# Optimization experiments

Measured on AMD Instinct MI355X. Metric: run time of the kernel, lower is better.

## Reference

```python
import jax, jax.numpy as jnp
import numpy as np

B, L, T, H, NH, NQ = 4096, 64, 48, 64, 4, 3
HD = H // NH  # head dim = 16


def lstm_layer(x, h0, c0, Wih, Whh, bih, bhh):
    # x: (B, S, I); h0, c0: (B, H). PyTorch gate order: i, f, g, o.
    def step(carry, xt):
        h, c = carry
        g = xt @ Wih.T + bih + h @ Whh.T + bhh
        i, f, gg, o = jnp.split(g, 4, axis=-1)
        c = jax.nn.sigmoid(f) * c + jax.nn.sigmoid(i) * jnp.tanh(gg)
        h = jax.nn.sigmoid(o) * jnp.tanh(c)
        return (h, c), h
    (hT, cT), hs = jax.lax.scan(step, (h0, c0), jnp.swapaxes(x, 0, 1))
    return jnp.swapaxes(hs, 0, 1), hT, cT


def lstm2(x, params, h0, c0):
    # params: list of 2 tuples (Wih, Whh, bih, bhh); h0, c0: (2, B, H)
    out = x
    hs, cs = [], []
    for l in range(2):
        Wih, Whh, bih, bhh = params[l]
        out, h, c = lstm_layer(out, h0[l], c0[l], Wih, Whh, bih, bhh)
        hs.append(h)
        cs.append(c)
    return out, jnp.stack(hs), jnp.stack(cs)


def mha(q, k, v, Wqkv, bqkv, Wo, bo):
    # PyTorch nn.MultiheadAttention, batch_first, averaged attn weights.
    Wq, Wk, Wv = jnp.split(Wqkv, 3, axis=0)
    bq, bk, bv = jnp.split(bqkv, 3, axis=0)
    def heads(t):
        b, s, _ = t.shape
        return t.reshape(b, s, NH, HD)
    qh = heads(q @ Wq.T + bq)
    kh = heads(k @ Wk.T + bk)
    vh = heads(v @ Wv.T + bv)
    scores = jnp.einsum('bqhd,bkhd->bhqk', qh, kh) / jnp.sqrt(jnp.float32(HD))
    w = jax.nn.softmax(scores, axis=-1)                      # (B, NH, Sq, Sk)
    out = jnp.einsum('bhqk,bkhd->bqhd', w, vh).reshape(q.shape[0], q.shape[1], H)
    return out @ Wo.T + bo, w.mean(axis=1)                   # averaged over heads


def setup_inputs() -> dict:
    key = jax.random.key(0)
    ks = iter(jax.random.split(key, 32))
    s = 0.08
    d = {
        'x': jax.random.normal(next(ks), (B, L, H), jnp.float32),
        'target': jax.random.normal(next(ks), (B, T, H), jnp.float32),
    }
    for pre in ('enc', 'dec'):
        for l in range(2):
            d[f'{pre}_Wih{l}'] = jax.random.normal(next(ks), (4 * H, H), jnp.float32) * s
            d[f'{pre}_Whh{l}'] = jax.random.normal(next(ks), (4 * H, H), jnp.float32) * s
            d[f'{pre}_bih{l}'] = jnp.zeros((4 * H,), jnp.float32)
            d[f'{pre}_bhh{l}'] = jnp.zeros((4 * H,), jnp.float32)
    d['attn_Wqkv'] = jax.random.normal(next(ks), (3 * H, H), jnp.float32) * s
    d['attn_bqkv'] = jnp.zeros((3 * H,), jnp.float32)
    d['attn_Wo'] = jax.random.normal(next(ks), (H, H), jnp.float32) * s
    d['attn_bo'] = jnp.zeros((H,), jnp.float32)
    d['fc_W1'] = jax.random.normal(next(ks), (H // 2, H), jnp.float32) * s
    d['fc_b1'] = jnp.zeros((H // 2,), jnp.float32)
    d['fc_W2'] = jax.random.normal(next(ks), (NQ, H // 2), jnp.float32) * s
    d['fc_b2'] = jnp.zeros((NQ,), jnp.float32)
    return d


def reference(x, target,
              enc_Wih0, enc_Whh0, enc_bih0, enc_bhh0,
              enc_Wih1, enc_Whh1, enc_bih1, enc_bhh1,
              dec_Wih0, dec_Whh0, dec_bih0, dec_bhh0,
              dec_Wih1, dec_Whh1, dec_bih1, dec_bhh1,
              attn_Wqkv, attn_bqkv, attn_Wo, attn_bo,
              fc_W1, fc_b1, fc_W2, fc_b2):
    enc_p = [(enc_Wih0, enc_Whh0, enc_bih0, enc_bhh0),
             (enc_Wih1, enc_Whh1, enc_bih1, enc_bhh1)]
    dec_p = [(dec_Wih0, dec_Whh0, dec_bih0, dec_bhh0),
             (dec_Wih1, dec_Whh1, dec_bih1, dec_bhh1)]
    z = jnp.zeros((2, x.shape[0], H), x.dtype)
    enc_out, h_n, c_n = lstm2(x, enc_p, z, z)               # (B, L, H)
    attn0, _ = mha(enc_out, enc_out, enc_out, attn_Wqkv, attn_bqkv, attn_Wo, attn_bo)
    # teacher forcing: step t>=1 consumes target[:, t-1]; step 0 the attended encoder summary
    dec_in = jnp.concatenate([attn0[:, -1:, :], target[:, :-1, :]], axis=1)  # (B, T, H)
    dec_out, _, _ = lstm2(dec_in, dec_p, h_n, c_n)          # (B, T, H)
    attn_out, attn_w = mha(dec_out, enc_out, enc_out, attn_Wqkv, attn_bqkv, attn_Wo, attn_bo)
    pred = jax.nn.relu(attn_out @ fc_W1.T + fc_b1) @ fc_W2.T + fc_b2  # (B, T, 3)
    return pred, attn_w                                      # (B,T,3), (B,T,L)
```

## Files before the change

### kernel.cpp

```cpp
#include <hip/hip_runtime.h>
#include <hip/hip_bf16.h>
#include <cstddef>


#define B_   4096
#define L_   64
#define T_   48
#define H_   64
#define ROWS 16
#define PADH 136
#define PADH2 72

using half8  = __attribute__((ext_vector_type(8))) _Float16;
using half4  = __attribute__((ext_vector_type(4))) _Float16;
using f32x4  = __attribute__((ext_vector_type(4))) float;

#define IC_ 4.8828125e-4f

__device__ __forceinline__ float fsig(float x) {
    return __builtin_amdgcn_rcpf(1.0f + __expf(-x));
}
__device__ __forceinline__ float ftanh(float x) {
    float e = __expf(-2.0f * fabsf(x));
    float r = (1.0f - e) * __builtin_amdgcn_rcpf(1.0f + e);
    return copysignf(r, x);
}

__global__ void transpose_w_all_kernel(
    const float* __restrict__ W0i, const float* __restrict__ W0h,
    const float* __restrict__ W1i, const float* __restrict__ W1h,
    const float* __restrict__ W2i, const float* __restrict__ W2h,
    const float* __restrict__ W3i, const float* __restrict__ W3h,
    _Float16* __restrict__ out) {
    int idx = blockIdx.x * 256 + threadIdx.x;
    int layer = idx >> 14, i = idx & 16383;
    const float* Wi = (layer == 0) ? W0i : (layer == 1) ? W1i : (layer == 2) ? W2i : W3i;
    const float* Wh = (layer == 0) ? W0h : (layer == 1) ? W1h : (layer == 2) ? W2h : W3h;
    int r = i >> 6, k = i & 63;
    _Float16* o = out + (size_t)layer * 32768;
    o[r * 128 + k]      = (_Float16)Wi[i];
    o[r * 128 + 64 + k] = (_Float16)Wh[i];
}

__global__ void split_aux_kernel(const float* __restrict__ Wqkv,
                                 const float* __restrict__ Wo,
                                 const float* __restrict__ W1,
                                 _Float16* __restrict__ wqkvh,
                                 _Float16* __restrict__ woh,
                                 _Float16* __restrict__ w1h,
                                 float* __restrict__ woT) {
    int idx = blockIdx.x * 256 + threadIdx.x;
    if (idx < 12288) {
        float v = Wqkv[idx]; _Float16 h = (_Float16)v;
        wqkvh[idx] = h; wqkvh[12288 + idx] = (_Float16)((v - (float)h) * 2048.f);
    } else if (idx < 16384) {
        int i = idx - 12288;
        float v = Wo[i]; _Float16 h = (_Float16)v;
        woh[i] = h; woh[4096 + i] = (_Float16)((v - (float)h) * 2048.f);
    } else if (idx < 18432) {
        int i = idx - 16384;
        float v = W1[i]; _Float16 h = (_Float16)v;
        w1h[i] = h; w1h[2048 + i] = (_Float16)((v - (float)h) * 2048.f);
    } else if (idx < 22528) {
        int i = idx - 18432; int r = i >> 6, k = i & 63;
        woT[k * 64 + r] = Wo[i];
    }
}

__global__ __launch_bounds__(512, 2) void lstm2_mfma_kernel(
    const float* __restrict__ inseq,
    const float* __restrict__ in0,
    const _Float16* __restrict__ w1half,
    const float* __restrict__ b1ihp, const float* __restrict__ b1hhp,
    const _Float16* __restrict__ w2half,
    const float* __restrict__ b2ihp, const float* __restrict__ b2hhp,
    const float* __restrict__ h01, const float* __restrict__ c01,
    const float* __restrict__ h02, const float* __restrict__ c02,
    _Float16* __restrict__ outh2,
    float* __restrict__ hf1, float* __restrict__ cf1,
    float* __restrict__ hf2, float* __restrict__ cf2,
    int S, int mode)
{
    __shared__ __align__(16) _Float16 A1[2][16 * PADH];
    __shared__ __align__(16) _Float16 A2h[2][16 * PADH2];

    const int tid  = threadIdx.x;
    const int w    = tid >> 6;
    const int lrow = tid & 15;
    const int lkg  = (tid >> 4) & 3;
    const int row0 = blockIdx.x * ROWS;

    const bool isL2w = (w >= 4);
    const int  wl    = w & 3;
    const int  hcol  = wl * 16 + lrow;

    const _Float16* wsrc = isL2w ? w2half : w1half;
    const float* bihp = isL2w ? b2ihp : b1ihp;
    const float* bhhp = isL2w ? b2hhp : b1hhp;

    half8 whi[4][4];
    #pragma unroll
    for (int kt = 0; kt < 4; ++kt)
        #pragma unroll
        for (int g = 0; g < 4; ++g) {
            const int col = g * 64 + hcol;
            whi[kt][g] = *(const half8*)&wsrc[(size_t)col * 128 + kt * 32 + lkg * 8];
        }
    float bsv[4];
    #pragma unroll
    for (int g = 0; g < 4; ++g)
        bsv[g] = bihp[g * 64 + hcol] + bhhp[g * 64 + hcol];

    float c[4], hlast[4] = {0.f, 0.f, 0.f, 0.f};

    const float* px[4];
    _Float16*    ph[4];

    if (!isL2w) {
        #pragma unroll
        for (int q = 0; q < 4; ++q) {
            const int r = 4 * lkg + q;
            const float* p0 = (mode == 1) ? (in0 + (size_t)(row0 + r) * 64)
                                          : (inseq + (size_t)(row0 + r) * S * 64);
            A1[0][r * PADH + hcol] = (_Float16)p0[hcol];
            float hv = h01 ? h01[(size_t)(row0 + r) * 64 + hcol] : 0.f;
            A1[0][r * PADH + 64 + hcol] = (_Float16)hv;
            c[q] = c01 ? c01[(size_t)(row0 + r) * 64 + hcol] : 0.f;
            px[q] = inseq + (size_t)(row0 + r) * S * 64 + hcol
                  + (mode == 1 ? 0 : 64);
        }
    } else {
        #pragma unroll
        for (int q = 0; q < 4; ++q) {
            const int r = 4 * lkg + q;
            float hv = h02 ? h02[(size_t)(row0 + r) * 64 + hcol] : 0.f;
            A2h[0][r * PADH2 + hcol] = (_Float16)hv;
            c[q] = c02 ? c02[(size_t)(row0 + r) * 64 + hcol] : 0.f;
            ph[q] = outh2 + (size_t)(row0 + r) * S * 64 + hcol;
        }
    }

    const int aoff = lrow * PADH + lkg * 8;

    for (int i = 0; i <= S; ++i) {
        asm volatile("s_waitcnt lgkmcnt(0)" ::: "memory");
        __builtin_amdgcn_s_barrier();
        __builtin_amdgcn_sched_barrier(0);

        if (!isL2w) {
            if (i < S) {
                float xn[4];
                if (i + 1 < S) {
                    #pragma unroll
                    for (int q = 0; q < 4; ++q) { xn[q] = *px[q]; px[q] += 64; }
                }
                const _Float16* As = A1[i & 1];
                f32x4 a0[4];
                #pragma unroll
                for (int g = 0; g < 4; ++g)
                    a0[g] = (f32x4){bsv[g], bsv[g], bsv[g], bsv[g]};
                #pragma unroll
                for (int kt = 0; kt < 4; ++kt) {
                    half8 ah = *(const half8*)&As[aoff + kt * 32];
                    #pragma unroll
                    for (int g = 0; g < 4; ++g)
                        a0[g] = __builtin_amdgcn_mfma_f32_16x16x32_f16(ah, whi[kt][g], a0[g], 0, 0, 0);
                }
                _Float16* Ad1 = A1[(i + 1) & 1];
                #pragma unroll
                for (int q = 0; q < 4; ++q) {
                    const int r = 4 * lkg + q;
                    float gi = a0[0][q], gf = a0[1][q], gg = a0[2][q], go = a0[3][q];
                    c[q] = fsig(gf) * c[q] + fsig(gi) * ftanh(gg);
                    float hv = fsig(go) * ftanh(c[q]);
                    hlast[q] = hv;
                    Ad1[r * PADH + 64 + hcol] = (_Float16)hv;
                }
                if (i + 1 < S) {
                    #pragma unroll
                    for (int q = 0; q < 4; ++q) {
                        const int r = 4 * lkg + q;
                        Ad1[r * PADH + hcol] = (_Float16)xn[q];
                    }
                }
            }
        } else {
            const int j = i - 1;
            if (j >= 0 && j < S) {
                const _Float16* Ah1 = A1[(j + 1) & 1];
                const _Float16* Ah2 = A2h[j & 1];
                f32x4 a0[4];
                #pragma unroll
                for (int g = 0; g < 4; ++g)
                    a0[g] = (f32x4){bsv[g], bsv[g], bsv[g], bsv[g]};
                #pragma unroll
                for (int kt = 0; kt < 2; ++kt) {
                    half8 ah = *(const half8*)&Ah1[lrow * PADH + 64 + kt * 32 + lkg * 8];
                    #pragma unroll
                    for (int g = 0; g < 4; ++g)
                        a0[g] = __builtin_amdgcn_mfma_f32_16x16x32_f16(ah, whi[kt][g], a0[g], 0, 0, 0);
                }
                #pragma unroll
                for (int kt = 2; kt < 4; ++kt) {
                    half8 ah = *(const half8*)&Ah2[lrow * PADH2 + (kt - 2) * 32 + lkg * 8];
                    #pragma unroll
                    for (int g = 0; g < 4; ++g)
                        a0[g] = __builtin_amdgcn_mfma_f32_16x16x32_f16(ah, whi[kt][g], a0[g], 0, 0, 0);
                }
                _Float16* Ad = A2h[(j + 1) & 1];
                #pragma unroll
                for (int q = 0; q < 4; ++q) {
                    const int r = 4 * lkg + q;
                    float gi = a0[0][q], gf = a0[1][q], gg = a0[2][q], go = a0[3][q];
                    c[q] = fsig(gf) * c[q] + fsig(gi) * ftanh(gg);
                    float hv = fsig(go) * ftanh(c[q]);
                    hlast[q] = hv;
                    _Float16 hh = (_Float16)hv;
                    Ad[r * PADH2 + hcol] = hh;
                    *ph[q] = hh; ph[q] += 64;
                }
            }
        }
    }
    if (hf1) {
        float* hdst = isL2w ? hf2 : hf1;
        float* cdst = isL2w ? cf2 : cf1;
        #pragma unroll
        for (int q = 0; q < 4; ++q) {
            const int r = 4 * lkg + q;
            hdst[(size_t)(row0 + r) * 64 + hcol] = hlast[q];
            cdst[(size_t)(row0 + r) * 64 + hcol] = c[q];
        }
    }
}

__global__ __launch_bounds__(256, 4) void attn0_v2(
    const _Float16* __restrict__ ench,
    const _Float16* __restrict__ wqkvh,
    const float* __restrict__ bqkv,
    const float* __restrict__ woT,
    const float* __restrict__ bo,
    float* __restrict__ a0last)
{
    __shared__ __align__(16) _Float16 E[64 * 72];
    __shared__ __align__(16) _Float16 K[64 * 72];
    __shared__ __align__(16) _Float16 V[64 * 72];
    __shared__ __align__(16) _Float16 Q[64 * 72];
    __shared__ float wsm[4 * 68];
    __shared__ float ov[64];
    __shared__ float part[4 * 64];

    const int b = blockIdx.x, tid = threadIdx.x;
    const int w = tid >> 6, l = tid & 63, lr = l & 15, lkg = l >> 4;

    {
        int row = tid >> 2, c0 = (tid & 3) * 16;
        const _Float16* ep = ench + (size_t)b * 4096 + row * 64 + c0;
        *(half8*)&E[row * 72 + c0]     = *(const half8*)ep;
        *(half8*)&E[row * 72 + c0 + 8] = *(const half8*)(ep + 8);
    }
    __syncthreads();

    for (int tt = w; tt < 12; tt += 4) {
        const int kind = tt >> 2;
        const int mrow = (tt & 3) * 16;
        const int wrowB = (kind == 0) ? 64 : ((kind == 1) ? 128 : 0);
        half8 ah[2];
        #pragma unroll
        for (int kt = 0; kt < 2; ++kt)
            ah[kt] = *(const half8*)&E[(mrow + lr) * 72 + kt * 32 + lkg * 8];
        _Float16* dst = (kind == 0) ? K : ((kind == 1) ? V : Q);
        #pragma unroll
        for (int nt = 0; nt < 4; ++nt) {
            const int col = nt * 16 + lr;
            const float bv = bqkv[wrowB + col];
            f32x4 a0 = (f32x4){bv, bv, bv, bv};
            #pragma unroll
            for (int kt = 0; kt < 2; ++kt) {
                half8 bh = *(const half8*)&wqkvh[(size_t)(wrowB + col) * 64 + kt * 32 + lkg * 8];
                a0 = __builtin_amdgcn_mfma_f32_16x16x32_f16(ah[kt], bh, a0, 0, 0, 0);
            }
            #pragma unroll
            for (int i = 0; i < 4; ++i)
                dst[(mrow + lkg * 4 + i) * 72 + col] = (_Float16)a0[i];
        }
    }
    __syncthreads();

    {
        const int kv = l;
        float s = 0.f;
        #pragma unroll
        for (int d = 0; d < 16; ++d)
            s += (float)Q[63 * 72 + w * 16 + d] * (float)K[kv * 72 + w * 16 + d];
        s *= 0.25f;
        float m = s;
        #pragma unroll
        for (int off = 32; off; off >>= 1) m = fmaxf(m, __shfl_xor(m, off));
        float e = __expf(s - m);
        float sum = e;
        #pragma unroll
        for (int off = 32; off; off >>= 1) sum += __shfl_xor(sum, off);
        wsm[w * 68 + kv] = e / sum;
    }
    __syncthreads();

    {
        const int d = l & 15, gr = l >> 4;
        float o = 0.f;
        #pragma unroll
        for (int k = 0; k < 16; ++k) {
            const int kv = gr * 16 + k;
            o += wsm[w * 68 + kv] * (float)V[kv * 72 + w * 16 + d];
        }
        o += __shfl_xor(o, 16);
        o += __shfl_xor(o, 32);
        if (l < 16) ov[w * 16 + l] = o;
    }
    __syncthreads();

    {
        const int j = tid & 63, g = tid >> 6;
        float p = 0.f;
        #pragma unroll
        for (int k = 0; k < 16; ++k) {
            const int kk = g * 16 + k;
            p += ov[kk] * woT[kk * 64 + j];
        }
        part[g * 64 + j] = p;
    }
    __syncthreads();
    if (tid < 64) {
        float a = bo[tid] + part[tid] + part[64 + tid] + part[128 + tid] + part[192 + tid];
        a0last[(size_t)b * 64 + tid] = a;
    }
}

__global__ __launch_bounds__(256, 4) void cross_attn_v3(
    const _Float16* __restrict__ ench, const _Float16* __restrict__ dech,
    const _Float16* __restrict__ wqkvh, const float* __restrict__ bqkv,
    const _Float16* __restrict__ woh,   const float* __restrict__ bo,
    const _Float16* __restrict__ w1h,   const float* __restrict__ b1,
    const float* __restrict__ W2,       const float* __restrict__ b2,
    float* __restrict__ pred, float* __restrict__ attnw)
{
    extern __shared__ __align__(16) char smem[];
    _Float16* E  = (_Float16*)(smem);
    _Float16* D  = (_Float16*)(smem + 9216);
    _Float16* K  = (_Float16*)(smem + 16128);
    _Float16* Q  = (_Float16*)(smem + 25344);
    _Float16* VT = (_Float16*)(smem + 32256);
    _Float16* AO = (_Float16*)(smem + 32256);
    float*    Hl = (float*)(smem + 32256);

    const int b = blockIdx.x, tid = threadIdx.x;
    const int w = tid >> 6, l = tid & 63, lr = l & 15, lkg = l >> 4;
    const int h = w;

    {
        int row = tid >> 2, c0 = (tid & 3) * 16;
        const _Float16* ep = ench + (size_t)b * 4096 + row * 64 + c0;
        *(half8*)&E[row * 72 + c0]     = *(const half8*)ep;
        *(half8*)&E[row * 72 + c0 + 8] = *(const half8*)(ep + 8);
        if (row < 48) {
            const _Float16* dp = dech + (size_t)b * 3072 + row * 64 + c0;
            *(half8*)&D[row * 72 + c0]     = *(const half8*)dp;
            *(half8*)&D[row * 72 + c0 + 8] = *(const half8*)(dp + 8);
        }
    }
    __syncthreads();

    for (int tt = w; tt < 11; tt += 4) {
        const int kind = (tt < 4) ? 0 : ((tt < 8) ? 1 : 2);
        const int mrow = ((kind == 0) ? tt : (kind == 1) ? tt - 4 : tt - 8) * 16;
        const int wrowB = (kind == 0) ? 64 : ((kind == 1) ? 128 : 0);
        const _Float16* S = (kind == 2) ? D : E;
        half8 ah[2];
        #pragma unroll
        for (int kt = 0; kt < 2; ++kt)
            ah[kt] = *(const half8*)&S[(mrow + lr) * 72 + kt * 32 + lkg * 8];
        #pragma unroll
        for (int nt = 0; nt < 4; ++nt) {
            const int col = nt * 16 + lr;
            const float bv = bqkv[wrowB + col];
            f32x4 a0 = (f32x4){bv, bv, bv, bv};
            #pragma unroll
            for (int kt = 0; kt < 2; ++kt) {
                half8 bh = *(const half8*)&wqkvh[(size_t)(wrowB + col) * 64 + kt * 32 + lkg * 8];
                a0 = __builtin_amdgcn_mfma_f32_16x16x32_f16(ah[kt], bh, a0, 0, 0, 0);
            }
            if (kind == 1) {
                half4 p;
                #pragma unroll
                for (int i = 0; i < 4; ++i) p[i] = (_Float16)a0[i];
                *(half4*)&VT[col * 68 + mrow + lkg * 4] = p;
            } else {
                _Float16* dst = (kind == 0) ? K : Q;
                #pragma unroll
                for (int i = 0; i < 4; ++i)
                    dst[(mrow + lkg * 4 + i) * 72 + col] = (_Float16)a0[i];
            }
        }
    }
    __syncthreads();

    const half8 z = {0, 0, 0, 0, 0, 0, 0, 0};
    half8 ka[4], qb[3];
    #pragma unroll
    for (int kvt = 0; kvt < 4; ++kvt)
        ka[kvt] = (lkg < 2) ? *(const half8*)&K[(kvt * 16 + lr) * 72 + h * 16 + lkg * 8] : z;
    #pragma unroll
    for (int qt = 0; qt < 3; ++qt)
        qb[qt] = (lkg < 2) ? *(const half8*)&Q[(qt * 16 + lr) * 72 + h * 16 + lkg * 8] : z;
    __syncthreads();

    _Float16* strip = (_Float16*)(smem + ((h == 0) ? 0 : (h == 1) ? 9216
                                        : (h == 2) ? 16128 : 25344));
    {
        f32x4 s[3][4];
        #pragma unroll
        for (int qt = 0; qt < 3; ++qt) {
            #pragma unroll
            for (int kvt = 0; kvt < 4; ++kvt) {
                f32x4 a0 = (f32x4){0.f, 0.f, 0.f, 0.f};
                a0 = __builtin_amdgcn_mfma_f32_16x16x32_f16(ka[kvt], qb[qt], a0, 0, 0, 0);
                s[qt][kvt] = a0 * 0.25f;
            }
            float m = s[qt][0][0];
            #pragma unroll
            for (int kvt = 0; kvt < 4; ++kvt)
                #pragma unroll
                for (int i = 0; i < 4; ++i) m = fmaxf(m, s[qt][kvt][i]);
            m = fmaxf(m, __shfl_xor(m, 16));
            m = fmaxf(m, __shfl_xor(m, 32));
            float sum = 0.f;
            #pragma unroll
            for (int kvt = 0; kvt < 4; ++kvt)
                #pragma unroll
                for (int i = 0; i < 4; ++i) {
                    float e = __expf(s[qt][kvt][i] - m);
                    s[qt][kvt][i] = e;
                    sum += e;
                }
            sum += __shfl_xor(sum, 16);
            sum += __shfl_xor(sum, 32);
            const float r = 1.0f / sum;
            #pragma unroll
            for (int kvt = 0; kvt < 4; ++kvt) {
                half4 p;
                #pragma unroll
                for (int i = 0; i < 4; ++i) p[i] = (_Float16)(s[qt][kvt][i] * r);
                *(half4*)&strip[(qt * 16 + lr) * 72 + kvt * 16 + lkg * 4] = p;
            }
        }
    }
    f32x4 pv[3];
    {
        half8 vb[2];
        #pragma unroll
        for (int kt = 0; kt < 2; ++kt) {
            half4 lo4 = *(const half4*)&VT[(h * 16 + lr) * 68 + kt * 32 + lkg * 8];
            half4 hi4 = *(const half4*)&VT[(h * 16 + lr) * 68 + kt * 32 + lkg * 8 + 4];
            #pragma unroll
            for (int j = 0; j < 4; ++j) { vb[kt][j] = lo4[j]; vb[kt][4 + j] = hi4[j]; }
        }
        #pragma unroll
        for (int qt = 0; qt < 3; ++qt) {
            f32x4 acc = (f32x4){0.f, 0.f, 0.f, 0.f};
            #pragma unroll
            for (int kt = 0; kt < 2; ++kt) {
                half8 wa = *(const half8*)&strip[(qt * 16 + lr) * 72 + kt * 32 + lkg * 8];
                acc = __builtin_amdgcn_mfma_f32_16x16x32_f16(wa, vb[kt], acc, 0, 0, 0);
            }
            pv[qt] = acc;
        }
    }
    __syncthreads();

    #pragma unroll
    for (int qt = 0; qt < 3; ++qt)
        #pragma unroll
        for (int i = 0; i < 4; ++i)
            AO[(qt * 16 + lkg * 4 + i) * 72 + h * 16 + lr] = (_Float16)pv[qt][i];
    __syncthreads();

    if (w < 3) {
        half8 bAO[2];
        #pragma unroll
        for (int kt = 0; kt < 2; ++kt)
            bAO[kt] = *(const half8*)&AO[(w * 16 + lr) * 72 + kt * 32 + lkg * 8];
        f32x4 ov[4];
        #pragma unroll
        for (int nt = 0; nt < 4; ++nt) {
            f32x4 acc = *(const f32x4*)&bo[nt * 16 + lkg * 4];
            #pragma unroll
            for (int kt = 0; kt < 2; ++kt) {
                half8 aW = *(const half8*)&woh[(size_t)(nt * 16 + lr) * 64 + kt * 32 + lkg * 8];
                acc = __builtin_amdgcn_mfma_f32_16x16x32_f16(aW, bAO[kt], acc, 0, 0, 0);
            }
            ov[nt] = acc;
        }
        #pragma unroll
        for (int nt = 0; nt < 4; ++nt) {
            half4 p;
            #pragma unroll
            for (int i = 0; i < 4; ++i) p[i] = (_Float16)ov[nt][i];
            *(half4*)&AO[(w * 16 + lr) * 72 + nt * 16 + lkg * 4] = p;
        }
        half8 bO[2];
        #pragma unroll
        for (int kt = 0; kt < 2; ++kt)
            bO[kt] = *(const half8*)&AO[(w * 16 + lr) * 72 + kt * 32 + lkg * 8];
        #pragma unroll
        for (int nt = 0; nt < 2; ++nt) {
            f32x4 acc = *(const f32x4*)&b1[nt * 16 + lkg * 4];
            #pragma unroll
            for (int kt = 0; kt < 2; ++kt) {
                half8 aW = *(const half8*)&w1h[(size_t)(nt * 16 + lr) * 64 + kt * 32 + lkg * 8];
                acc = __builtin_amdgcn_mfma_f32_16x16x32_f16(aW, bO[kt], acc, 0, 0, 0);
            }
            f32x4 rl;
            #pragma unroll
            for (int i = 0; i < 4; ++i) rl[i] = fmaxf(acc[i], 0.f);
            *(f32x4*)&Hl[(w * 16 + lr) * 36 + nt * 16 + lkg * 4] = rl;
        }
        if (l < 48) {
            const int qr = l / 3, n = l - 3 * qr;
            const int q = w * 16 + qr;
            float a = b2[n];
            #pragma unroll
            for (int m2 = 0; m2 < 32; ++m2) a += Hl[q * 36 + m2] * W2[n * 32 + m2];
            pred[((size_t)b * 48 + q) * 3 + n] = a;
        }
    } else {
        const _Float16* s0 = (const _Float16*)(smem);
        const _Float16* s1 = (const _Float16*)(smem + 9216);
        const _Float16* s2 = (const _Float16*)(smem + 16128);
        const _Float16* s3 = (const _Float16*)(smem + 25344);
        #pragma unroll 4
        for (int it = 0; it < 48; ++it) {
            int idx = l + it * 64;
            int o = (idx >> 6) * 72 + (idx & 63);
            attnw[(size_t)b * 3072 + idx] =
                0.25f * ((float)s0[o] + (float)s1[o] + (float)s2[o] + (float)s3[o]);
        }
    }
}

extern "C" void kernel_launch(void* const* d_in, const int* in_sizes, int n_in,
                              void* d_out, int out_size, void* d_ws, size_t ws_size,
                              hipStream_t stream) {
    const float* x      = (const float*)d_in[0];
    const float* target = (const float*)d_in[1];
    const float* eWih0 = (const float*)d_in[2],  *eWhh0 = (const float*)d_in[3];
    const float* ebih0 = (const float*)d_in[4],  *ebhh0 = (const float*)d_in[5];
    const float* eWih1 = (const float*)d_in[6],  *eWhh1 = (const float*)d_in[7];
    const float* ebih1 = (const float*)d_in[8],  *ebhh1 = (const float*)d_in[9];
    const float* dWih0 = (const float*)d_in[10], *dWhh0 = (const float*)d_in[11];
    const float* dbih0 = (const float*)d_in[12], *dbhh0 = (const float*)d_in[13];
    const float* dWih1 = (const float*)d_in[14], *dWhh1 = (const float*)d_in[15];
    const float* dbih1 = (const float*)d_in[16], *dbhh1 = (const float*)d_in[17];
    const float* Wqkv = (const float*)d_in[18], *bqkv = (const float*)d_in[19];
    const float* Wo   = (const float*)d_in[20], *bo   = (const float*)d_in[21];
    const float* W1   = (const float*)d_in[22], *b1   = (const float*)d_in[23];
    const float* W2   = (const float*)d_in[24], *b2   = (const float*)d_in[25];

    float* ws = (float*)d_ws;
    float* hseq1  = ws;
    float* encout = hseq1  + (size_t)B_ * L_ * H_;
    float* decout = encout + (size_t)B_ * L_ * H_;
    float* a0last = decout + (size_t)B_ * T_ * H_;
    float* hfin   = a0last + (size_t)B_ * H_;
    float* cfin   = hfin   + (size_t)2 * B_ * H_;
    float* wtg    = cfin   + (size_t)2 * B_ * H_;
    float* auxw   = wtg    + (size_t)4 * 32768;

    _Float16* wh0 = (_Float16*)(wtg);
    _Float16* wh1 = wh0 + 32768;
    _Float16* wh2 = wh1 + 32768;
    _Float16* wh3 = wh2 + 32768;
    _Float16* wqkvh = (_Float16*)auxw;
    _Float16* woh   = wqkvh + 24576;
    _Float16* w1h   = woh + 8192;
    float*    woT   = auxw + 18432;
    _Float16* encouth = (_Float16*)hseq1;
    _Float16* decouth = encouth + (size_t)B_ * L_ * H_;

    float* pred  = (float*)d_out;
    float* attnw = pred + (size_t)B_ * T_ * 3;

    transpose_w_all_kernel<<<256, 256, 0, stream>>>(
        eWih0, eWhh0, eWih1, eWhh1, dWih0, dWhh0, dWih1, dWhh1, wh0);
    split_aux_kernel<<<88, 256, 0, stream>>>(Wqkv, Wo, W1, wqkvh, woh, w1h, woT);

    lstm2_mfma_kernel<<<B_ / ROWS, 512, 0, stream>>>(
        x, nullptr, wh0, ebih0, ebhh0, wh1, ebih1, ebhh1,
        nullptr, nullptr, nullptr, nullptr,
        encouth, hfin, cfin, hfin + (size_t)B_ * H_, cfin + (size_t)B_ * H_,
        L_, 0);
    attn0_v2<<<B_, 256, 0, stream>>>(encouth, wqkvh, bqkv, woT, bo, a0last);
    lstm2_mfma_kernel<<<B_ / ROWS, 512, 0, stream>>>(
        target, a0last, wh2, dbih0, dbhh0, wh3, dbih1, dbhh1,
        hfin, cfin, hfin + (size_t)B_ * H_, cfin + (size_t)B_ * H_,
        decouth, nullptr, nullptr, nullptr, nullptr, T_, 1);
    cross_attn_v3<<<B_, 256, 40960, stream>>>(
        encouth, decouth, wqkvh, bqkv, woh, bo, w1h, b1, W2, b2, pred, attnw);
}
```

Before: 256.3 us.

## Widen cross-attention block to 8 waves splitting query tiles across halves

The cross-attention kernel goes from 256 to 512 threads per batch row. The second group of four waves takes the third query tile of each head's score, softmax and PV work, and also helps with the loads and projection tiles. The goal is to shorten the per-block critical path by spreading work over more waves. In exchange, the 4:3 split is uneven, the extra waves sit idle in the later output stages, and launch bounds of (512,1) may limit how many blocks share a CU.

```diff
diff --git a/kernel.cpp b/kernel.cpp
--- a/kernel.cpp
+++ b/kernel.cpp
@@ -14,8 +14,6 @@
 using half8  = __attribute__((ext_vector_type(8))) _Float16;
 using half4  = __attribute__((ext_vector_type(4))) _Float16;
 using f32x4  = __attribute__((ext_vector_type(4))) float;
-
-#define IC_ 4.8828125e-4f
 
 __device__ __forceinline__ float fsig(float x) {
     return __builtin_amdgcn_rcpf(1.0f + __expf(-x));
@@ -336,7 +334,52 @@
     }
 }
 
-__global__ __launch_bounds__(256, 4) void cross_attn_v3(
+__device__ __forceinline__ f32x4 score_pv_one(
+    int qt, half8 qbq, const half8* ka, _Float16* strip,
+    half8 vb0, half8 vb1, int lr, int lkg)
+{
+    f32x4 s[4];
+    #pragma unroll
+    for (int kvt = 0; kvt < 4; ++kvt) {
+        f32x4 a0 = (f32x4){0.f, 0.f, 0.f, 0.f};
+        a0 = __builtin_amdgcn_mfma_f32_16x16x32_f16(ka[kvt], qbq, a0, 0, 0, 0);
+        s[kvt] = a0 * 0.25f;
+    }
+    float m = s[0][0];
+    #pragma unroll
+    for (int kvt = 0; kvt < 4; ++kvt)
+        #pragma unroll
+        for (int i = 0; i < 4; ++i) m = fmaxf(m, s[kvt][i]);
+    m = fmaxf(m, __shfl_xor(m, 16));
+    m = fmaxf(m, __shfl_xor(m, 32));
+    float sum = 0.f;
+    #pragma unroll
+    for (int kvt = 0; kvt < 4; ++kvt)
+        #pragma unroll
+        for (int i = 0; i < 4; ++i) {
+            float e = __expf(s[kvt][i] - m);
+            s[kvt][i] = e;
+            sum += e;
+        }
+    sum += __shfl_xor(sum, 16);
+    sum += __shfl_xor(sum, 32);
+    const float r = 1.0f / sum;
+    #pragma unroll
+    for (int kvt = 0; kvt < 4; ++kvt) {
+        half4 p;
+        #pragma unroll
+        for (int i = 0; i < 4; ++i) p[i] = (_Float16)(s[kvt][i] * r);
+        *(half4*)&strip[(qt * 16 + lr) * 72 + kvt * 16 + lkg * 4] = p;
+    }
+    f32x4 acc = (f32x4){0.f, 0.f, 0.f, 0.f};
+    half8 wa0 = *(const half8*)&strip[(qt * 16 + lr) * 72 + 0 + lkg * 8];
+    acc = __builtin_amdgcn_mfma_f32_16x16x32_f16(wa0, vb0, acc, 0, 0, 0);
+    half8 wa1 = *(const half8*)&strip[(qt * 16 + lr) * 72 + 32 + lkg * 8];
+    acc = __builtin_amdgcn_mfma_f32_16x16x32_f16(wa1, vb1, acc, 0, 0, 0);
+    return acc;
+}
+
+__global__ __launch_bounds__(512, 1) void cross_attn_v5(
     const _Float16* __restrict__ ench, const _Float16* __restrict__ dech,
     const _Float16* __restrict__ wqkvh, const float* __restrict__ bqkv,
     const _Float16* __restrict__ woh,   const float* __restrict__ bo,
@@ -355,22 +398,19 @@
 
     const int b = blockIdx.x, tid = threadIdx.x;
     const int w = tid >> 6, l = tid & 63, lr = l & 15, lkg = l >> 4;
-    const int h = w;
+    const int h = w & 3, half = w >> 2;
 
     {
-        int row = tid >> 2, c0 = (tid & 3) * 16;
-        const _Float16* ep = ench + (size_t)b * 4096 + row * 64 + c0;
-        *(half8*)&E[row * 72 + c0]     = *(const half8*)ep;
-        *(half8*)&E[row * 72 + c0 + 8] = *(const half8*)(ep + 8);
-        if (row < 48) {
-            const _Float16* dp = dech + (size_t)b * 3072 + row * 64 + c0;
-            *(half8*)&D[row * 72 + c0]     = *(const half8*)dp;
-            *(half8*)&D[row * 72 + c0 + 8] = *(const half8*)(dp + 8);
-        }
-    }
-    __syncthreads();
-
-    for (int tt = w; tt < 11; tt += 4) {
+        const int row = tid >> 3, c0 = (tid & 7) * 8;
+        *(half8*)&E[row * 72 + c0] =
+            *(const half8*)(ench + (size_t)b * 4096 + row * 64 + c0);
+        if (tid < 384)
+            *(half8*)&D[row * 72 + c0] =
+                *(const half8*)(dech + (size_t)b * 3072 + row * 64 + c0);
+    }
+    __syncthreads();
+
+    for (int tt = w; tt < 11; tt += 8) {
         const int kind = (tt < 4) ? 0 : ((tt < 8) ? 1 : 2);
         const int mrow = ((kind == 0) ? tt : (kind == 1) ? tt - 4 : tt - 8) * 16;
         const int wrowB = (kind == 0) ? 64 : ((kind == 1) ? 128 : 0);
@@ -405,83 +445,54 @@
     __syncthreads();
 
     const half8 z = {0, 0, 0, 0, 0, 0, 0, 0};
-    half8 ka[4], qb[3];
+    half8 ka[4];
     #pragma unroll
     for (int kvt = 0; kvt < 4; ++kvt)
         ka[kvt] = (lkg < 2) ? *(const half8*)&K[(kvt * 16 + lr) * 72 + h * 16 + lkg * 8] : z;
-    #pragma unroll
-    for (int qt = 0; qt < 3; ++qt)
-        qb[qt] = (lkg < 2) ? *(const half8*)&Q[(qt * 16 + lr) * 72 + h * 16 + lkg * 8] : z;
+    half8 qbA = z, qbB = z;
+    if (lkg < 2) {
+        if (!half) {
+            qbA = *(const half8*)&Q[(0 + lr) * 72 + h * 16 + lkg * 8];
+            qbB = *(const half8*)&Q[(16 + lr) * 72 + h * 16 + lkg * 8];
+        } else {
+            qbA = *(const half8*)&Q[(32 + lr) * 72 + h * 16 + lkg * 8];
+        }
+    }
     __syncthreads();
 
     _Float16* strip = (_Float16*)(smem + ((h == 0) ? 0 : (h == 1) ? 9216
                                         : (h == 2) ? 16128 : 25344));
+    half8 vb0, vb1;
     {
-        f32x4 s[3][4];
-        #pragma unroll
-        for (int qt = 0; qt < 3; ++qt) {
-            #pragma unroll
-            for (int kvt = 0; kvt < 4; ++kvt) {
-                f32x4 a0 = (f32x4){0.f, 0.f, 0.f, 0.f};
-                a0 = __builtin_amdgcn_mfma_f32_16x16x32_f16(ka[kvt], qb[qt], a0, 0, 0, 0);
-                s[qt][kvt] = a0 * 0.25f;
-            }
-            float m = s[qt][0][0];
-            #pragma unroll
-            for (int kvt = 0; kvt < 4; ++kvt)
-                #pragma unroll
-                for (int i = 0; i < 4; ++i) m = fmaxf(m, s[qt][kvt][i]);
-            m = fmaxf(m, __shfl_xor(m, 16));
-            m = fmaxf(m, __shfl_xor(m, 32));
-            float sum = 0.f;
-            #pragma unroll
-            for (int kvt = 0; kvt < 4; ++kvt)
-                #pragma unroll
-                for (int i = 0; i < 4; ++i) {
-                    float e = __expf(s[qt][kvt][i] - m);
-                    s[qt][kvt][i] = e;
-                    sum += e;
-                }
-            sum += __shfl_xor(sum, 16);
-            sum += __shfl_xor(sum, 32);
-            const float r = 1.0f / sum;
-            #pragma unroll
-            for (int kvt = 0; kvt < 4; ++kvt) {
-                half4 p;
-                #pragma unroll
-                for (int i = 0; i < 4; ++i) p[i] = (_Float16)(s[qt][kvt][i] * r);
-                *(half4*)&strip[(qt * 16 + lr) * 72 + kvt * 16 + lkg * 4] = p;
-            }
-        }
-    }
-    f32x4 pv[3];
-    {
-        half8 vb[2];
-        #pragma unroll
-        for (int kt = 0; kt < 2; ++kt) {
-            half4 lo4 = *(const half4*)&VT[(h * 16 + lr) * 68 + kt * 32 + lkg * 8];
-            half4 hi4 = *(const half4*)&VT[(h * 16 + lr) * 68 + kt * 32 + lkg * 8 + 4];
-            #pragma unroll
-            for (int j = 0; j < 4; ++j) { vb[kt][j] = lo4[j]; vb[kt][4 + j] = hi4[j]; }
-        }
-        #pragma unroll
-        for (int qt = 0; qt < 3; ++qt) {
-            f32x4 acc = (f32x4){0.f, 0.f, 0.f, 0.f};
-            #pragma unroll
-            for (int kt = 0; kt < 2; ++kt) {
-                half8 wa = *(const half8*)&strip[(qt * 16 + lr) * 72 + kt * 32 + lkg * 8];
-                acc = __builtin_amdgcn_mfma_f32_16x16x32_f16(wa, vb[kt], acc, 0, 0, 0);
-            }
-            pv[qt] = acc;
-        }
-    }
-    __syncthreads();
-
-    #pragma unroll
-    for (int qt = 0; qt < 3; ++qt)
+        half4 lo4 = *(const half4*)&VT[(h * 16 + lr) * 68 + 0 + lkg * 8];
+        half4 hi4 = *(const half4*)&VT[(h * 16 + lr) * 68 + 0 + lkg * 8 + 4];
+        #pragma unroll
+        for (int j = 0; j < 4; ++j) { vb0[j] = lo4[j]; vb0[4 + j] = hi4[j]; }
+        lo4 = *(const half4*)&VT[(h * 16 + lr) * 68 + 32 + lkg * 8];
+        hi4 = *(const half4*)&VT[(h * 16 + lr) * 68 + 32 + lkg * 8 + 4];
+        #pragma unroll
+        for (int j = 0; j < 4; ++j) { vb1[j] = lo4[j]; vb1[4 + j] = hi4[j]; }
+    }
+    f32x4 pvA, pvB;
+    if (!half) {
+        pvA = score_pv_one(0, qbA, ka, strip, vb0, vb1, lr, lkg);
+        pvB = score_pv_one(1, qbB, ka, strip, vb0, vb1, lr, lkg);
+    } else {
+        pvA = score_pv_one(2, qbA, ka, strip, vb0, vb1, lr, lkg);
+    }
+    __syncthreads();
+
+    if (!half) {
+        #pragma unroll
+        for (int i = 0; i < 4; ++i) {
+            AO[(0 + lkg * 4 + i) * 72 + h * 16 + lr]  = (_Float16)pvA[i];
+            AO[(16 + lkg * 4 + i) * 72 + h * 16 + lr] = (_Float16)pvB[i];
+        }
+    } else {
         #pragma unroll
         for (int i = 0; i < 4; ++i)
-            AO[(qt * 16 + lkg * 4 + i) * 72 + h * 16 + lr] = (_Float16)pv[qt][i];
+            AO[(32 + lkg * 4 + i) * 72 + h * 16 + lr] = (_Float16)pvA[i];
+    }
     __syncthreads();
 
     if (w < 3) {
@@ -532,7 +543,7 @@
             for (int m2 = 0; m2 < 32; ++m2) a += Hl[q * 36 + m2] * W2[n * 32 + m2];
             pred[((size_t)b * 48 + q) * 3 + n] = a;
         }
-    } else {
+    } else if (w == 3) {
         const _Float16* s0 = (const _Float16*)(smem);
         const _Float16* s1 = (const _Float16*)(smem + 9216);
         const _Float16* s2 = (const _Float16*)(smem + 16128);
@@ -603,6 +614,6 @@
         target, a0last, wh2, dbih0, dbhh0, wh3, dbih1, dbhh1,
         hfin, cfin, hfin + (size_t)B_ * H_, cfin + (size_t)B_ * H_,
         decouth, nullptr, nullptr, nullptr, nullptr, T_, 1);
-    cross_attn_v3<<<B_, 256, 40960, stream>>>(
+    cross_attn_v5<<<B_, 512, 40960, stream>>>(
         encouth, decouth, wqkvh, bqkv, woh, bo, w1h, b1, W2, b2, pred, attnw);
 }
```

After: 260.9 us. About the same (+1.8%).
